# Kernel optimization log

Measured on AMD Instinct MI355X. Metric: run time of the kernel, lower is better.

## Reference

```python
import jax, jax.numpy as jnp
import numpy as np

DIM, H, KVH = 1024, 16, 4
HD = DIM // H            # head_dim = 64
KV_DIM = KVH * HD        # 256
ROPE_BASE = 10000.0
EPS = 1e-6


def setup_inputs() -> dict:
    key = jax.random.key(0)
    ks = jax.random.split(key, 6)
    B, S = 4, 2048
    x = jax.random.normal(ks[0], (B, S, DIM), dtype=jnp.float32)
    sc = 0.02
    Wq = jax.random.normal(ks[1], (DIM, DIM), dtype=jnp.float32) * sc
    Wk = jax.random.normal(ks[2], (KV_DIM, DIM), dtype=jnp.float32) * sc
    Wv = jax.random.normal(ks[3], (KV_DIM, DIM), dtype=jnp.float32) * sc
    Wo = jax.random.normal(ks[4], (DIM, DIM), dtype=jnp.float32) * sc
    q_gain = jnp.full((H,), 1.5, dtype=jnp.float32)
    return {"x": x, "Wq": Wq, "Wk": Wk, "Wv": Wv, "Wo": Wo, "q_gain": q_gain}


def _rms_norm(t):
    return t * jax.lax.rsqrt(jnp.mean(t * t, axis=-1, keepdims=True) + EPS)


def _rotary(seqlen, dtype):
    inv_freq = 1.0 / (ROPE_BASE ** (jnp.arange(0, HD, 2, dtype=jnp.float32) / HD))
    t = jnp.arange(seqlen, dtype=jnp.float32)
    freqs = jnp.outer(t, inv_freq)                      # [S, HD/2]
    return jnp.cos(freqs).astype(dtype)[None, None], jnp.sin(freqs).astype(dtype)[None, None]


def _apply_rot(t, cos, sin):
    half = t.shape[-1] // 2
    t1, t2 = t[..., :half], t[..., half:]
    return jnp.concatenate((t1 * cos + t2 * sin, -t1 * sin + t2 * cos), axis=-1)


def reference(x, Wq, Wk, Wv, Wo, q_gain):
    B, S, D = x.shape
    q = (x @ Wq.T).reshape(B, S, H, HD).transpose(0, 2, 1, 3)      # [B,H,S,HD]
    k = (x @ Wk.T).reshape(B, S, KVH, HD).transpose(0, 2, 1, 3)    # [B,KVH,S,HD]
    v = (x @ Wv.T).reshape(B, S, KVH, HD).transpose(0, 2, 1, 3)
    q, k = _rms_norm(q), _rms_norm(k)
    cos, sin = _rotary(S, q.dtype)
    q, k = _apply_rot(q, cos, sin), _apply_rot(k, cos, sin)
    q = q * q_gain.astype(q.dtype)[None, :, None, None]
    rep = H // KVH
    k_exp = jnp.repeat(k, rep, axis=1)                              # GQA expand
    v_exp = jnp.repeat(v, rep, axis=1)
    scores = jnp.einsum('bhqd,bhkd->bhqk', q, k_exp) / np.sqrt(HD)
    causal = jnp.tril(jnp.ones((S, S), dtype=bool))
    scores = jnp.where(causal[None, None], scores, jnp.finfo(scores.dtype).min)
    attn = jax.nn.softmax(scores, axis=-1)
    y = jnp.einsum('bhqk,bhkd->bhqd', attn, v_exp)
    y = y.transpose(0, 2, 1, 3).reshape(B, S, D)
    return y @ Wo.T
```

## Files before the change

kernel.cpp:

```cpp
#include <hip/hip_runtime.h>

typedef float f32x4 __attribute__((ext_vector_type(4)));
typedef float f32x16 __attribute__((ext_vector_type(16)));
typedef __bf16 bf16x8 __attribute__((ext_vector_type(8)));
typedef unsigned short u16x8 __attribute__((ext_vector_type(8)));
typedef int i32x2 __attribute__((ext_vector_type(2)));
typedef int i32x4 __attribute__((ext_vector_type(4)));

#define DEV static __device__ __forceinline__

DEV float bf2f(unsigned short h) {
  unsigned int u = ((unsigned int)h) << 16;
  return __builtin_bit_cast(float, u);
}
DEV unsigned short f2bf(float f) {
  unsigned int u = __builtin_bit_cast(unsigned int, f);
  u += 0x7fff + ((u >> 16) & 1);
  return (unsigned short)(u >> 16);
}

DEV void g2l16(const void* g, void* l) {
  __builtin_amdgcn_global_load_lds(
      (const __attribute__((address_space(1))) void*)g,
      (__attribute__((address_space(3))) void*)l, 16, 0, 0);
}

DEV unsigned int cvtpk(float lo, float hi) {
  unsigned int r;
  asm("v_cvt_pk_bf16_f32 %0, %1, %2" : "=v"(r) : "v"(lo), "v"(hi));
  return r;
}

DEV void cvt8(const float* __restrict__ in, unsigned short* __restrict__ out, int idx) {
  int i = idx * 8;
  float4 a = *(const float4*)(in + i);
  float4 b = *(const float4*)(in + i + 4);
  u16x8 r;
  r[0] = f2bf(a.x); r[1] = f2bf(a.y); r[2] = f2bf(a.z); r[3] = f2bf(a.w);
  r[4] = f2bf(b.x); r[5] = f2bf(b.y); r[6] = f2bf(b.z); r[7] = f2bf(b.w);
  *(u16x8*)(out + i) = r;
}

__global__ __launch_bounds__(256) void k_cvt_all(const float* __restrict__ x,
                                                 const float* __restrict__ wq,
                                                 const float* __restrict__ wk,
                                                 const float* __restrict__ wv,
                                                 const float* __restrict__ wo,
                                                 unsigned short* __restrict__ xb,
                                                 unsigned short* __restrict__ wcat,
                                                 unsigned short* __restrict__ wob,
                                                 float2* __restrict__ rope) {
  const int blk = blockIdx.x, tid = threadIdx.x;
  if (blk < 4096) {
    cvt8(x, xb, blk * 256 + tid);
  } else if (blk < 4608) {
    cvt8(wq, wcat, (blk - 4096) * 256 + tid);
  } else if (blk < 4736) {
    cvt8(wk, wcat + 1048576, (blk - 4608) * 256 + tid);
  } else if (blk < 4864) {
    cvt8(wv, wcat + 1310720, (blk - 4736) * 256 + tid);
  } else if (blk < 5376) {
    cvt8(wo, wob, (blk - 4864) * 256 + tid);
  } else {
    int idx = (blk - 5376) * 256 + tid;
    int s = idx >> 5, dmod = idx & 31;
    float inv_freq = powf(10000.0f, -(float)dmod * (1.0f / 32.0f));
    float sn, cs;
    sincosf((float)s * inv_freq, &sn, &cs);
    rope[idx] = make_float2(cs, sn);
  }
}

__global__ __launch_bounds__(256) void k_qkv(const unsigned short* __restrict__ A,
                                             const unsigned short* __restrict__ B,
                                             const float* __restrict__ qg,
                                             const float2* __restrict__ rope,
                                             unsigned short* __restrict__ qn,
                                             unsigned short* __restrict__ kn,
                                             unsigned short* __restrict__ vt) {
  __shared__ unsigned short LDS[16384];
  unsigned short* As = LDS;
  unsigned short* Bs = LDS + 8192;
  const int K = 1024;
  const int tid = threadIdx.x;
  const int wid = tid >> 6, lane = tid & 63;
  const int g = lane >> 4, r16 = lane & 15;
  const int m0 = blockIdx.x * 128;
  const int y = blockIdx.y;
  const int n0 = y * 128;
  const int wr = wid >> 1, wc = wid & 1;

  f32x4 acc[4][4];
#pragma unroll
  for (int i = 0; i < 4; ++i)
#pragma unroll
    for (int j = 0; j < 4; ++j) acc[i][j] = f32x4{0.f, 0.f, 0.f, 0.f};

  const int cb = (lane & 7) * 16;

  for (int k0 = 0; k0 < K; k0 += 64) {
#pragma unroll
    for (int c = 0; c < 4; ++c) {
      int i = wid * 4 + c;
      int row = i * 8 + (lane >> 3);
      int sc = cb ^ ((row & 7) << 4);
      g2l16((const char*)A + ((size_t)(m0 + row) * K + k0) * 2 + sc, (char*)As + i * 1024);
      g2l16((const char*)B + ((size_t)(n0 + row) * K + k0) * 2 + sc, (char*)Bs + i * 1024);
    }
    __syncthreads();
#pragma unroll
    for (int kh = 0; kh < 2; ++kh) {
      bf16x8 af[4], bfr[4];
#pragma unroll
      for (int m = 0; m < 4; ++m) {
        int row = wr * 64 + m * 16 + r16;
        int byte = row * 128 + ((g * 16 + kh * 64) ^ ((row & 7) << 4));
        af[m] = *(const bf16x8*)((const char*)As + byte);
      }
#pragma unroll
      for (int n = 0; n < 4; ++n) {
        int row = wc * 64 + n * 16 + r16;
        int byte = row * 128 + ((g * 16 + kh * 64) ^ ((row & 7) << 4));
        bfr[n] = *(const bf16x8*)((const char*)Bs + byte);
      }
#pragma unroll
      for (int m = 0; m < 4; ++m)
#pragma unroll
        for (int n = 0; n < 4; ++n)
          acc[m][n] = __builtin_amdgcn_mfma_f32_16x16x32_bf16(af[m], bfr[n], acc[m][n], 0, 0, 0);
    }
    __syncthreads();
  }

  if (y < 10) {
    const bool isq = (y < 8);
    const int head = isq ? (2 * y + wc) : (2 * (y - 8) + wc);
    const float gain = isq ? qg[head] * 0.18033688011112042f : 1.0f;
#pragma unroll
    for (int m = 0; m < 4; ++m)
#pragma unroll
      for (int j = 0; j < 4; ++j) {
        int rowl = wr * 64 + m * 16 + g * 4 + j;
        int tok = m0 + rowl;
        int s = tok & 2047;
        float v0 = acc[m][0][j], v1 = acc[m][1][j], v2 = acc[m][2][j], v3 = acc[m][3][j];
        float ss = v0 * v0 + v1 * v1 + v2 * v2 + v3 * v3;
        ss += __shfl_xor(ss, 1); ss += __shfl_xor(ss, 2);
        ss += __shfl_xor(ss, 4); ss += __shfl_xor(ss, 8);
        float rs = rsqrtf(ss * (1.0f / 64.0f) + 1e-6f) * gain;
        float2 cs0 = rope[s * 32 + r16];
        float2 cs1 = rope[s * 32 + 16 + r16];
        float o0 = (v0 * cs0.x + v2 * cs0.y) * rs;
        float o2 = (v2 * cs0.x - v0 * cs0.y) * rs;
        float o1 = (v1 * cs1.x + v3 * cs1.y) * rs;
        float o3 = (v3 * cs1.x - v1 * cs1.y) * rs;
        unsigned short* dst = isq ? (qn + (size_t)tok * 1024 + head * 64)
                                  : (kn + (size_t)tok * 256 + head * 64);
        dst[r16] = f2bf(o0);
        dst[16 + r16] = f2bf(o1);
        dst[32 + r16] = f2bf(o2);
        dst[48 + r16] = f2bf(o3);
      }
  } else {
    unsigned short* T = LDS;
#pragma unroll
    for (int m = 0; m < 4; ++m)
#pragma unroll
      for (int n = 0; n < 4; ++n)
#pragma unroll
        for (int j = 0; j < 4; ++j) {
          int tokl = wr * 64 + m * 16 + g * 4 + j;
          int dl = wc * 64 + n * 16 + r16;
          int byte = (dl * 256 + tokl * 2) ^ ((dl & 15) << 4);
          *(unsigned short*)((char*)T + byte) = f2bf(acc[m][n][j]);
        }
    __syncthreads();
    const int d = tid >> 1, th = tid & 1;
    const int hv = 2 * (y - 10) + (d >> 6), dh = d & 63;
    const int bb = m0 >> 11;
    const int s0 = (m0 & 2047) + th * 64;
    unsigned short* dstv = vt + ((size_t)(bb * 4 + hv) * 64 + dh) * 2048 + s0;
    const int swz = (d & 15) << 4;
#pragma unroll
    for (int c = 0; c < 8; ++c) {
      i32x4 w = *(const i32x4*)((const char*)T + ((d * 256 + th * 128 + c * 16) ^ swz));
      *(i32x4*)(dstv + c * 8) = w;
    }
  }
}

__global__ __launch_bounds__(256) void k_gemm_bt(const unsigned short* __restrict__ A,
                                                 const unsigned short* __restrict__ B,
                                                 float* __restrict__ C, int M, int N, int K) {
  __shared__ unsigned short As[128 * 64];
  __shared__ unsigned short Bs[128 * 64];
  const int tid = threadIdx.x;
  const int wid = tid >> 6, lane = tid & 63;
  const int g = lane >> 4, r16 = lane & 15;
  const int m0 = blockIdx.x * 128, n0 = blockIdx.y * 128;
  const int wr = wid >> 1, wc = wid & 1;

  f32x4 acc[4][4];
#pragma unroll
  for (int i = 0; i < 4; ++i)
#pragma unroll
    for (int j = 0; j < 4; ++j) acc[i][j] = f32x4{0.f, 0.f, 0.f, 0.f};

  const int cb = (lane & 7) * 16;

  for (int k0 = 0; k0 < K; k0 += 64) {
#pragma unroll
    for (int c = 0; c < 4; ++c) {
      int i = wid * 4 + c;
      int row = i * 8 + (lane >> 3);
      int sc = cb ^ ((row & 7) << 4);
      g2l16((const char*)A + ((size_t)(m0 + row) * K + k0) * 2 + sc, (char*)As + i * 1024);
      g2l16((const char*)B + ((size_t)(n0 + row) * K + k0) * 2 + sc, (char*)Bs + i * 1024);
    }
    __syncthreads();
#pragma unroll
    for (int kh = 0; kh < 2; ++kh) {
      bf16x8 af[4], bfr[4];
#pragma unroll
      for (int m = 0; m < 4; ++m) {
        int row = wr * 64 + m * 16 + r16;
        int byte = row * 128 + ((g * 16 + kh * 64) ^ ((row & 7) << 4));
        af[m] = *(const bf16x8*)((const char*)As + byte);
      }
#pragma unroll
      for (int n = 0; n < 4; ++n) {
        int row = wc * 64 + n * 16 + r16;
        int byte = row * 128 + ((g * 16 + kh * 64) ^ ((row & 7) << 4));
        bfr[n] = *(const bf16x8*)((const char*)Bs + byte);
      }
#pragma unroll
      for (int m = 0; m < 4; ++m)
#pragma unroll
        for (int n = 0; n < 4; ++n)
          acc[m][n] = __builtin_amdgcn_mfma_f32_16x16x32_bf16(af[m], bfr[n], acc[m][n], 0, 0, 0);
    }
    __syncthreads();
  }
#pragma unroll
  for (int m = 0; m < 4; ++m)
#pragma unroll
    for (int n = 0; n < 4; ++n)
#pragma unroll
      for (int j = 0; j < 4; ++j) {
        int row = m0 + wr * 64 + m * 16 + g * 4 + j;
        int col = n0 + wc * 64 + n * 16 + r16;
        C[(size_t)row * N + col] = acc[m][n][j];
      }
}

__global__ __launch_bounds__(256) void k_attn2(const unsigned short* __restrict__ qn,
                                               const unsigned short* __restrict__ kn,
                                               const unsigned short* __restrict__ vt,
                                               unsigned short* __restrict__ yb) {
  __shared__ unsigned short SMEM[2 * 8192];
  const int tid = threadIdx.x;
  const int wid = tid >> 6, lane = tid & 63;
  const int hi = lane >> 5, l31 = lane & 31;
  const int flat = blockIdx.x;
  const int qx = 15 - (flat >> 6);
  const int bh = flat & 63;
  const int b = bh >> 4, h = bh & 15, hv = h >> 2;
  const int q0w = qx * 128 + wid * 32;
  const int qglob = q0w + l31;
  const size_t tok0 = (size_t)b * 2048;
  const unsigned short* vtb = vt + (size_t)(b * 4 + hv) * 64 * 2048;

  const u16x8 onesu = {0x3F80, 0x3F80, 0x3F80, 0x3F80, 0x3F80, 0x3F80, 0x3F80, 0x3F80};
  const bf16x8 ones = __builtin_bit_cast(bf16x8, onesu);

  bf16x8 qf[4];
#pragma unroll
  for (int m = 0; m < 4; ++m)
    qf[m] = *(const bf16x8*)(qn + (tok0 + qglob) * 1024 + h * 64 + m * 16 + hi * 8);

  f32x16 oacc[2], lacc, zer;
#pragma unroll
  for (int r = 0; r < 16; ++r) { oacc[0][r] = 0.f; oacc[1][r] = 0.f; lacc[r] = 0.f; zer[r] = 0.f; }

  const int nt = qx * 2 + 2;

  auto stage = [&](int T, int buf) {
    unsigned short* KsB = SMEM + buf * 8192;
    unsigned short* VtB = KsB + 4096;
    const int kk0 = T * 64;
#pragma unroll
    for (int c = 0; c < 2; ++c) {
      int i = wid * 2 + c;
      int row = i * 8 + (lane >> 3);
      int sc = ((lane & 7) * 16) ^ ((row & 7) << 4);
      g2l16((const char*)(kn + (tok0 + kk0 + row) * 256 + hv * 64) + sc, (char*)KsB + i * 1024);
      g2l16((const char*)(vtb + (size_t)row * 2048 + kk0) + sc, (char*)VtB + i * 1024);
    }
  };

  auto tile = [&](int t, int buf) {
    const int k0 = t * 64;
    if (t + 1 < nt) stage(t + 1, buf ^ 1);

    if (k0 <= q0w + 31) {
      const unsigned short* KsB = SMEM + buf * 8192;
      const unsigned short* VtB = KsB + 4096;
      f32x16 s[2];
#pragma unroll
      for (int kt = 0; kt < 2; ++kt) {
        const int krow = kt * 32 + l31;
        const char* kbase = (const char*)KsB + krow * 128;
        const int ksw = (krow & 7) << 4;
        __builtin_amdgcn_s_setprio(1);
        bf16x8 kf = *(const bf16x8*)(kbase + ((0 * 32 + hi * 16) ^ ksw));
        f32x16 acc = __builtin_amdgcn_mfma_f32_32x32x16_bf16(kf, qf[0], zer, 0, 0, 0);
#pragma unroll
        for (int m = 1; m < 4; ++m) {
          kf = *(const bf16x8*)(kbase + ((m * 32 + hi * 16) ^ ksw));
          acc = __builtin_amdgcn_mfma_f32_32x32x16_bf16(kf, qf[m], acc, 0, 0, 0);
        }
        __builtin_amdgcn_s_setprio(0);
        s[kt] = acc;
      }
      if (k0 + 63 > q0w) {
#pragma unroll
        for (int kt = 0; kt < 2; ++kt)
#pragma unroll
          for (int r = 0; r < 16; ++r) {
            int key = k0 + kt * 32 + (r & 3) + 8 * (r >> 2) + 4 * hi;
            if (key > qglob) s[kt][r] = -INFINITY;
          }
      }
#pragma unroll
      for (int kt = 0; kt < 2; ++kt)
#pragma unroll
        for (int r = 0; r < 16; ++r) s[kt][r] = exp2f(s[kt][r]);
      i32x4 paw[4];
#pragma unroll
      for (int kt = 0; kt < 2; ++kt)
#pragma unroll
        for (int half = 0; half < 2; ++half) {
          int bs = half * 8;
          unsigned int a0 = cvtpk(s[kt][bs + 0], s[kt][bs + 1]);
          unsigned int a1 = cvtpk(s[kt][bs + 2], s[kt][bs + 3]);
          unsigned int b0 = cvtpk(s[kt][bs + 4], s[kt][bs + 5]);
          unsigned int b1 = cvtpk(s[kt][bs + 6], s[kt][bs + 7]);
          i32x2 r0 = __builtin_amdgcn_permlane32_swap((int)a0, (int)b0, false, false);
          i32x2 r1 = __builtin_amdgcn_permlane32_swap((int)a1, (int)b1, false, false);
          i32x4 w;
          w[0] = r0[0]; w[1] = r1[0]; w[2] = r0[1]; w[3] = r1[1];
          paw[kt * 2 + half] = w;
        }
      __builtin_amdgcn_s_setprio(1);
#pragma unroll
      for (int db = 0; db < 2; ++db) {
        const int vrow = db * 32 + l31;
        const char* vbase = (const char*)VtB + vrow * 128;
        const int vsw = (vrow & 7) << 4;
#pragma unroll
        for (int ks = 0; ks < 4; ++ks) {
          bf16x8 vf = *(const bf16x8*)(vbase + ((ks * 32 + hi * 16) ^ vsw));
          oacc[db] = __builtin_amdgcn_mfma_f32_32x32x16_bf16(
              vf, __builtin_bit_cast(bf16x8, paw[ks]), oacc[db], 0, 0, 0);
        }
      }
#pragma unroll
      for (int ks = 0; ks < 4; ++ks)
        lacc = __builtin_amdgcn_mfma_f32_32x32x16_bf16(
            ones, __builtin_bit_cast(bf16x8, paw[ks]), lacc, 0, 0, 0);
      __builtin_amdgcn_s_setprio(0);
    }
    __syncthreads();
  };

  stage(0, 0);
  __syncthreads();
  for (int tt = 0; tt < nt; tt += 2) {
    tile(tt, 0);
    tile(tt + 1, 1);
  }

  const float inv = 1.0f / lacc[0];
  const int swl = (l31 & 7) << 4;
  char* obase = (char*)SMEM + wid * 4096;
#pragma unroll
  for (int db = 0; db < 2; ++db)
#pragma unroll
    for (int i = 0; i < 8; ++i) {
      int r = 2 * i;
      int dim = db * 32 + (r & 3) + 8 * (r >> 2) + 4 * hi;
      unsigned int w = (unsigned int)f2bf(oacc[db][r] * inv) |
                       ((unsigned int)f2bf(oacc[db][r + 1] * inv) << 16);
      *(unsigned int*)(obase + l31 * 128 + ((dim * 2) ^ swl)) = w;
    }
  __syncthreads();
#pragma unroll
  for (int it = 0; it < 4; ++it) {
    int cc = it * 2 + hi;
    i32x4 w = *(const i32x4*)(obase + l31 * 128 + ((cc * 16) ^ swl));
    *(i32x4*)(yb + (tok0 + q0w + l31) * 1024 + h * 64 + cc * 8) = w;
  }
}

extern "C" void kernel_launch(void* const* d_in, const int* in_sizes, int n_in,
                              void* d_out, int out_size, void* d_ws, size_t ws_size,
                              hipStream_t stream) {
  (void)in_sizes; (void)n_in; (void)out_size; (void)ws_size;
  const float* x  = (const float*)d_in[0];
  const float* Wq = (const float*)d_in[1];
  const float* Wk = (const float*)d_in[2];
  const float* Wv = (const float*)d_in[3];
  const float* Wo = (const float*)d_in[4];
  const float* qg = (const float*)d_in[5];

  char* ws = (char*)d_ws;
  unsigned short* xb   = (unsigned short*)(ws);
  unsigned short* wcat = (unsigned short*)(ws + 16777216);
  unsigned short* wob  = (unsigned short*)(ws + 19922944);
  unsigned short* qn   = (unsigned short*)(ws + 22020096);
  unsigned short* kn   = (unsigned short*)(ws + 38797312);
  unsigned short* yb   = xb;
  unsigned short* vt   = (unsigned short*)((char*)d_out + 25165824);
  float2*         rope = (float2*)((char*)d_out + 29360128);

  k_cvt_all<<<5632, 256, 0, stream>>>(x, Wq, Wk, Wv, Wo, xb, wcat, wob, rope);
  k_qkv<<<dim3(64, 12), 256, 0, stream>>>(xb, wcat, qg, rope, qn, kn, vt);
  k_attn2<<<1024, 256, 0, stream>>>(qn, kn, vt, yb);
  k_gemm_bt<<<dim3(64, 8), 256, 0, stream>>>(yb, wob, (float*)d_out, 8192, 1024, 1024);
}
```

Before: 154.6 us.

## Process KV tiles in pairs with four-buffer staging and hoisted causal masking

The attention loop now handles two 64-key tiles per iteration and prefetches the next pair into a four-buffer LDS ring. This halves the number of barriers and lets the QK MFMAs for both tiles be issued together, overlapping with softmax. Causal masking runs only on the final diagonal pair, so the per-tile branch checks are gone. The cost is double the LDS footprint (64KB), which may reduce occupancy, plus more live registers for the two score sets. Warps whose rows lie entirely below the diagonal tiles no longer skip those tiles.

```diff
diff --git a/kernel.cpp b/kernel.cpp
--- a/kernel.cpp
+++ b/kernel.cpp
@@ -257,7 +257,7 @@
                                                const unsigned short* __restrict__ kn,
                                                const unsigned short* __restrict__ vt,
                                                unsigned short* __restrict__ yb) {
-  __shared__ unsigned short SMEM[2 * 8192];
+  __shared__ unsigned short SMEM[4 * 8192];
   const int tid = threadIdx.x;
   const int wid = tid >> 6, lane = tid & 63;
   const int hi = lane >> 5, l31 = lane & 31;
@@ -282,10 +282,8 @@
 #pragma unroll
   for (int r = 0; r < 16; ++r) { oacc[0][r] = 0.f; oacc[1][r] = 0.f; lacc[r] = 0.f; zer[r] = 0.f; }
 
-  const int nt = qx * 2 + 2;
-
-  auto stage = [&](int T, int buf) {
-    unsigned short* KsB = SMEM + buf * 8192;
+  auto stage = [&](int T, int tb) {
+    unsigned short* KsB = SMEM + tb * 8192;
     unsigned short* VtB = KsB + 4096;
     const int kk0 = T * 64;
 #pragma unroll
@@ -298,86 +296,117 @@
     }
   };
 
-  auto tile = [&](int t, int buf) {
+  auto qk_tile = [&](int tb, f32x16* s) {
+    const char* kbase0 = (const char*)SMEM + tb * 16384;
+#pragma unroll
+    for (int kt = 0; kt < 2; ++kt) {
+      const int krow = kt * 32 + l31;
+      const char* kbase = kbase0 + krow * 128;
+      const int ksw = (krow & 7) << 4;
+      __builtin_amdgcn_s_setprio(1);
+      bf16x8 kf = *(const bf16x8*)(kbase + ((hi * 16) ^ ksw));
+      f32x16 a = __builtin_amdgcn_mfma_f32_32x32x16_bf16(kf, qf[0], zer, 0, 0, 0);
+#pragma unroll
+      for (int m = 1; m < 4; ++m) {
+        kf = *(const bf16x8*)(kbase + ((m * 32 + hi * 16) ^ ksw));
+        a = __builtin_amdgcn_mfma_f32_32x32x16_bf16(kf, qf[m], a, 0, 0, 0);
+      }
+      __builtin_amdgcn_s_setprio(0);
+      s[kt] = a;
+    }
+  };
+
+  auto mask_tile = [&](int t, f32x16* s) {
     const int k0 = t * 64;
-    if (t + 1 < nt) stage(t + 1, buf ^ 1);
-
-    if (k0 <= q0w + 31) {
-      const unsigned short* KsB = SMEM + buf * 8192;
-      const unsigned short* VtB = KsB + 4096;
-      f32x16 s[2];
-#pragma unroll
-      for (int kt = 0; kt < 2; ++kt) {
-        const int krow = kt * 32 + l31;
-        const char* kbase = (const char*)KsB + krow * 128;
-        const int ksw = (krow & 7) << 4;
-        __builtin_amdgcn_s_setprio(1);
-        bf16x8 kf = *(const bf16x8*)(kbase + ((0 * 32 + hi * 16) ^ ksw));
-        f32x16 acc = __builtin_amdgcn_mfma_f32_32x32x16_bf16(kf, qf[0], zer, 0, 0, 0);
-#pragma unroll
-        for (int m = 1; m < 4; ++m) {
-          kf = *(const bf16x8*)(kbase + ((m * 32 + hi * 16) ^ ksw));
-          acc = __builtin_amdgcn_mfma_f32_32x32x16_bf16(kf, qf[m], acc, 0, 0, 0);
-        }
-        __builtin_amdgcn_s_setprio(0);
-        s[kt] = acc;
-      }
-      if (k0 + 63 > q0w) {
-#pragma unroll
-        for (int kt = 0; kt < 2; ++kt)
-#pragma unroll
-          for (int r = 0; r < 16; ++r) {
-            int key = k0 + kt * 32 + (r & 3) + 8 * (r >> 2) + 4 * hi;
-            if (key > qglob) s[kt][r] = -INFINITY;
-          }
-      }
-#pragma unroll
-      for (int kt = 0; kt < 2; ++kt)
-#pragma unroll
-        for (int r = 0; r < 16; ++r) s[kt][r] = exp2f(s[kt][r]);
-      i32x4 paw[4];
-#pragma unroll
-      for (int kt = 0; kt < 2; ++kt)
-#pragma unroll
-        for (int half = 0; half < 2; ++half) {
-          int bs = half * 8;
-          unsigned int a0 = cvtpk(s[kt][bs + 0], s[kt][bs + 1]);
-          unsigned int a1 = cvtpk(s[kt][bs + 2], s[kt][bs + 3]);
-          unsigned int b0 = cvtpk(s[kt][bs + 4], s[kt][bs + 5]);
-          unsigned int b1 = cvtpk(s[kt][bs + 6], s[kt][bs + 7]);
-          i32x2 r0 = __builtin_amdgcn_permlane32_swap((int)a0, (int)b0, false, false);
-          i32x2 r1 = __builtin_amdgcn_permlane32_swap((int)a1, (int)b1, false, false);
-          i32x4 w;
-          w[0] = r0[0]; w[1] = r1[0]; w[2] = r0[1]; w[3] = r1[1];
-          paw[kt * 2 + half] = w;
-        }
-      __builtin_amdgcn_s_setprio(1);
-#pragma unroll
-      for (int db = 0; db < 2; ++db) {
-        const int vrow = db * 32 + l31;
-        const char* vbase = (const char*)VtB + vrow * 128;
-        const int vsw = (vrow & 7) << 4;
-#pragma unroll
-        for (int ks = 0; ks < 4; ++ks) {
-          bf16x8 vf = *(const bf16x8*)(vbase + ((ks * 32 + hi * 16) ^ vsw));
-          oacc[db] = __builtin_amdgcn_mfma_f32_32x32x16_bf16(
-              vf, __builtin_bit_cast(bf16x8, paw[ks]), oacc[db], 0, 0, 0);
-        }
-      }
-#pragma unroll
-      for (int ks = 0; ks < 4; ++ks)
-        lacc = __builtin_amdgcn_mfma_f32_32x32x16_bf16(
-            ones, __builtin_bit_cast(bf16x8, paw[ks]), lacc, 0, 0, 0);
-      __builtin_amdgcn_s_setprio(0);
-    }
-    __syncthreads();
+#pragma unroll
+    for (int kt = 0; kt < 2; ++kt)
+#pragma unroll
+      for (int r = 0; r < 16; ++r) {
+        int key = k0 + kt * 32 + (r & 3) + 8 * (r >> 2) + 4 * hi;
+        if (key > qglob) s[kt][r] = -INFINITY;
+      }
   };
 
+  auto softmax_cvt = [&](f32x16* s, i32x4* paw) {
+#pragma unroll
+    for (int kt = 0; kt < 2; ++kt)
+#pragma unroll
+      for (int r = 0; r < 16; ++r) s[kt][r] = exp2f(s[kt][r]);
+#pragma unroll
+    for (int kt = 0; kt < 2; ++kt)
+#pragma unroll
+      for (int half = 0; half < 2; ++half) {
+        int bs = half * 8;
+        unsigned int a0 = cvtpk(s[kt][bs + 0], s[kt][bs + 1]);
+        unsigned int a1 = cvtpk(s[kt][bs + 2], s[kt][bs + 3]);
+        unsigned int b0 = cvtpk(s[kt][bs + 4], s[kt][bs + 5]);
+        unsigned int b1 = cvtpk(s[kt][bs + 6], s[kt][bs + 7]);
+        i32x2 r0 = __builtin_amdgcn_permlane32_swap((int)a0, (int)b0, false, false);
+        i32x2 r1 = __builtin_amdgcn_permlane32_swap((int)a1, (int)b1, false, false);
+        i32x4 w;
+        w[0] = r0[0]; w[1] = r1[0]; w[2] = r0[1]; w[3] = r1[1];
+        paw[kt * 2 + half] = w;
+      }
+  };
+
+  auto pv_tile = [&](int tb, const i32x4* paw) {
+    const char* vbase0 = (const char*)SMEM + tb * 16384 + 8192;
+    __builtin_amdgcn_s_setprio(1);
+#pragma unroll
+    for (int db = 0; db < 2; ++db) {
+      const int vrow = db * 32 + l31;
+      const char* vbase = vbase0 + vrow * 128;
+      const int vsw = (vrow & 7) << 4;
+#pragma unroll
+      for (int ks = 0; ks < 4; ++ks) {
+        bf16x8 vf = *(const bf16x8*)(vbase + ((ks * 32 + hi * 16) ^ vsw));
+        oacc[db] = __builtin_amdgcn_mfma_f32_32x32x16_bf16(
+            vf, __builtin_bit_cast(bf16x8, paw[ks]), oacc[db], 0, 0, 0);
+      }
+    }
+#pragma unroll
+    for (int ks = 0; ks < 4; ++ks)
+      lacc = __builtin_amdgcn_mfma_f32_32x32x16_bf16(
+          ones, __builtin_bit_cast(bf16x8, paw[ks]), lacc, 0, 0, 0);
+    __builtin_amdgcn_s_setprio(0);
+  };
+
+  const int npair = qx + 1;
+
   stage(0, 0);
+  stage(1, 1);
   __syncthreads();
-  for (int tt = 0; tt < nt; tt += 2) {
-    tile(tt, 0);
-    tile(tt + 1, 1);
+
+  for (int p = 0; p < npair - 1; ++p) {
+    const int pb = (p & 1) << 1;
+    const int nb = pb ^ 2;
+    stage(2 * p + 2, nb);
+    stage(2 * p + 3, nb | 1);
+    f32x16 sa[2], sb[2];
+    qk_tile(pb, sa);
+    qk_tile(pb | 1, sb);
+    i32x4 pawa[4], pawb[4];
+    softmax_cvt(sa, pawa);
+    pv_tile(pb, pawa);
+    softmax_cvt(sb, pawb);
+    pv_tile(pb | 1, pawb);
+    __syncthreads();
+  }
+  {
+    const int p = npair - 1;
+    const int pb = (p & 1) << 1;
+    const int t0 = 2 * p;
+    f32x16 sa[2], sb[2];
+    qk_tile(pb, sa);
+    qk_tile(pb | 1, sb);
+    mask_tile(t0, sa);
+    mask_tile(t0 + 1, sb);
+    i32x4 pawa[4], pawb[4];
+    softmax_cvt(sa, pawa);
+    pv_tile(pb, pawa);
+    softmax_cvt(sb, pawb);
+    pv_tile(pb | 1, pawb);
+    __syncthreads();
   }
 
   const float inv = 1.0f / lacc[0];
```

Result: no change. 151.9 us (-1.7%).
